# Performance work log

Hardware: AMD Instinct MI355X
Metric: run time of the kernel (lower is better)

The kernel has to match this reference:

```python
import jax, jax.numpy as jnp
import numpy as np

N, D = 4096, 512
TAU, ALPHA, EPS = 0.2, 0.5, 1e-15
L2_EPS = 1e-12  # F.normalize eps


def setup_inputs() -> dict:
    key = jax.random.key(0)
    ks = jax.random.split(key, 12)
    # xavier_normal_ with gain=1.414 for [D, D] linears
    std = 1.414 * (2.0 / (D + D)) ** 0.5
    xn = lambda k: jax.random.normal(k, (D, D), jnp.float32) * std
    return {
        "z1": jax.random.normal(ks[0], (N, D), jnp.float32),
        "z2": jax.random.normal(ks[1], (N, D), jnp.float32),
        # local projector: Linear -> PReLU -> Linear
        "lw1": xn(ks[2]), "lb1": jnp.zeros((D,), jnp.float32),
        "la": jnp.full((1,), 0.25, jnp.float32),  # PReLU weight (torch default 0.25)
        "lw2": xn(ks[3]), "lb2": jnp.zeros((D,), jnp.float32),
        # global projector
        "gw1": xn(ks[4]), "gb1": jnp.zeros((D,), jnp.float32),
        "ga": jnp.full((1,), 0.25, jnp.float32),
        "gw2": xn(ks[5]), "gb2": jnp.zeros((D,), jnp.float32),
        # discriminator bilinear weight
        "W": xn(ks[6]),
        # binary positive-pair mask [N, N]
        "mask": jax.random.randint(ks[7], (N, N), 0, 2, jnp.int32),
    }


def _prelu(x, a):
    return jnp.where(x >= 0, x, a * x)


def _proj(z, w1, b1, a, w2, b2):
    # nn.Sequential(Linear, PReLU, Linear); torch Linear: z @ W.T + b
    return _prelu(z @ w1.T + b1, a[0]) @ w2.T + b2


def _l2norm(z):
    n = jnp.linalg.norm(z, axis=-1, keepdims=True)
    return z / jnp.maximum(n, L2_EPS)


def _infonce(h1, h2, m, tau):
    a = _l2norm(h1)
    b = _l2norm(h2)
    sim_intra = jnp.exp(a @ a.T / tau)  # [N, N]
    sim_inter = jnp.exp(a @ b.T / tau)  # [N, N]
    num = (sim_inter * m).sum(1)
    den = sim_intra.sum(1) + sim_inter.sum(1) - (sim_intra * m).sum(1)
    return (-jnp.log(num / den)).mean()


def reference(z1, z2, lw1, lb1, la, lw2, lb2, gw1, gb1, ga, gw2, gb2, W, mask):
    m = mask.astype(jnp.float32)
    # local (node-level) InfoNCE through the local projector
    h1 = _proj(z1, lw1, lb1, la, lw2, lb2)
    h2 = _proj(z2, lw1, lb1, la, lw2, lb2)
    local = 0.5 * (_infonce(h1, h2, m, TAU) + _infonce(h2, h1, m.T, TAU))

    # global (DGI-style) loss
    def gloss(pos_z, neg_z):
        s = pos_z.mean(0)                               # readout [D]
        h = _proj(s, gw1, gb1, ga, gw2, gb2)            # global projector [D]
        summ = W @ h                                    # [D]
        d_pos = jax.nn.sigmoid(pos_z @ summ)            # [N]
        d_neg = jax.nn.sigmoid(neg_z @ summ)            # [N]
        pos_loss = -jnp.log(d_pos + EPS).mean()
        neg_loss = -jnp.log(1.0 - d_neg + EPS).mean()
        return 0.5 * (pos_loss + neg_loss)

    glob = 0.5 * (gloss(z1, z2) + gloss(z2, z1))
    return ALPHA * local + (1.0 - ALPHA) * glob
```

## Files before the change

### kernel.cpp

```cpp
#include <hip/hip_runtime.h>
#include <math.h>

#define NN 4096
#define DD 512
#define INV_TAU 5.0f
#define EPSV 1e-15f

typedef unsigned short u16;
typedef __attribute__((ext_vector_type(8))) short short8;
typedef __attribute__((ext_vector_type(4))) float f32x4;

__device__ __forceinline__ void gld16(const void* g, void* l) {
  __builtin_amdgcn_global_load_lds(
      (const __attribute__((address_space(1))) unsigned int*)g,
      (__attribute__((address_space(3))) unsigned int*)l, 16, 0, 0);
}

__device__ __forceinline__ float bf2f(u16 u) {
  return __uint_as_float(((unsigned)u) << 16);
}
__device__ __forceinline__ u16 f2bf(float x) {
  unsigned u = __float_as_uint(x);
  u += 0x7fff + ((u >> 16) & 1);
  return (u16)(u >> 16);
}

__device__ __forceinline__ float wave_sum(float v) {
#pragma unroll
  for (int o = 32; o > 0; o >>= 1) v += __shfl_down(v, o, 64);
  return v;
}

__global__ __launch_bounds__(256) void tobf16_2(const float* __restrict__ a,
                                                const float* __restrict__ b,
                                                u16* __restrict__ d,
                                                int n4each) {
  const int i = blockIdx.x * 256 + threadIdx.x;
  const float* s =
      (i < n4each) ? a + (size_t)i * 4 : b + (size_t)(i - n4each) * 4;
  float4 v = *(const float4*)s;
  unsigned long long pk = (unsigned long long)f2bf(v.x) |
                          ((unsigned long long)f2bf(v.y) << 16) |
                          ((unsigned long long)f2bf(v.z) << 32) |
                          ((unsigned long long)f2bf(v.w) << 48);
  *(unsigned long long*)&d[(size_t)i * 4] = pk;
}

template <int ACT>
__global__ __launch_bounds__(256) void gemm_mfma(
    const u16* __restrict__ A, const u16* __restrict__ Bw,
    const float* __restrict__ bias, const float* __restrict__ alpha_p,
    u16* __restrict__ out) {
  __shared__ __align__(16) u16 sA[2][128 * 32], sB[2][128 * 32];
  const int tid = threadIdx.x, w = tid >> 6, lane = tid & 63;
  const int rq = lane >> 2, cq = (lane & 3) * 8;
  const int quad = lane >> 4, m16 = lane & 15;
  const int wi = w >> 1, wj = w & 1;
  const int i0 = blockIdx.y * 128, j0 = blockIdx.x * 128;
  const u16* Ab = A + (size_t)blockIdx.z * ((size_t)NN * DD);
  u16* ob = out + (size_t)blockIdx.z * ((size_t)NN * DD);
  const int p = w >> 1, rh = (w & 1) * 64;
  const u16* gs = p ? Bw : Ab;
  const int grow0 = (p ? j0 : i0) + rh + rq;
  u16* lb0 = p ? &sB[0][rh * 32] : &sA[0][rh * 32];
  u16* lb1 = p ? &sB[1][rh * 32] : &sA[1][rh * 32];
#pragma unroll
  for (int rr = 0; rr < 64; rr += 16)
    gld16(&gs[(size_t)(grow0 + rr) * DD + cq], lb0 + rr * 32);
  f32x4 acc[4][4] = {};
  for (int kc = 0; kc < 16; ++kc) {
    __syncthreads();
    if (kc < 15) {
      const int kn = (kc + 1) * 32;
      u16* d = (kc & 1) ? lb0 : lb1;
#pragma unroll
      for (int rr = 0; rr < 64; rr += 16)
        gld16(&gs[(size_t)(grow0 + rr) * DD + kn + cq], d + rr * 32);
    }
    const u16* As = sA[kc & 1];
    const u16* Bs = sB[kc & 1];
    short8 ar[4], br[4];
#pragma unroll
    for (int s = 0; s < 4; ++s) {
      ar[s] = *(const short8*)&As[(wi * 64 + s * 16 + m16) * 32 + quad * 8];
      br[s] = *(const short8*)&Bs[(wj * 64 + s * 16 + m16) * 32 + quad * 8];
    }
#pragma unroll
    for (int si = 0; si < 4; ++si)
#pragma unroll
      for (int sj = 0; sj < 4; ++sj)
        acc[si][sj] = __builtin_amdgcn_mfma_f32_16x16x32_bf16(
            ar[si], br[sj], acc[si][sj], 0, 0, 0);
  }
  const float al = ACT ? alpha_p[0] : 0.f;
#pragma unroll
  for (int si = 0; si < 4; ++si)
#pragma unroll
    for (int sj = 0; sj < 4; ++sj) {
      const int col = j0 + wj * 64 + sj * 16 + m16;
      const float bv = bias[col];
#pragma unroll
      for (int r = 0; r < 4; ++r) {
        const int row = i0 + wi * 64 + si * 16 + quad * 4 + r;
        float x = acc[si][sj][r] + bv;
        if (ACT) x = (x >= 0.f) ? x : al * x;
        ob[(size_t)row * DD + col] = f2bf(x);
      }
    }
}

__global__ __launch_bounds__(256) void rownorm_bf16(const u16* __restrict__ h,
                                                    u16* __restrict__ o) {
  const int row = blockIdx.x;
  const int t = threadIdx.x;
  const size_t base = (size_t)row * DD;
  float v0 = bf2f(h[base + t]);
  float v1 = bf2f(h[base + 256 + t]);
  float s = v0 * v0 + v1 * v1;
  s = wave_sum(s);
  __shared__ float wsum[4];
  const int lane = t & 63, wid = t >> 6;
  if (lane == 0) wsum[wid] = s;
  __syncthreads();
  if (t == 0) {
    float tot = wsum[0] + wsum[1] + wsum[2] + wsum[3];
    wsum[0] = 1.f / fmaxf(sqrtf(tot), 1e-12f);
  }
  __syncthreads();
  const float inv = wsum[0];
  o[base + t] = f2bf(v0 * inv);
  o[base + 256 + t] = f2bf(v1 * inv);
}

__global__ __launch_bounds__(512) void sim_mfma(
    const u16* __restrict__ na, const u16* __restrict__ nb,
    const int* __restrict__ mask, float* __restrict__ zb) {
  __shared__ __align__(16) u16 sP[2][4][128 * 32];
  const int tid = threadIdx.x;
  const int w = tid >> 6, lane = tid & 63;
  const int rq = lane >> 2, cq = (lane & 3) * 8;
  const int quad = lane >> 4, m16 = lane & 15;
  const int ig = w & 3, jh = w >> 2;
  const int i0 = blockIdx.y * 128, j0 = blockIdx.x * 128;
  const int p = w >> 1, rh = (w & 1) * 64;
  const u16* gs = (p & 1) ? nb : na;
  const int grow0 = ((p < 2) ? i0 : j0) + rh + rq;
  u16* lb0 = &sP[0][p][rh * 32];
  u16* lb1 = &sP[1][p][rh * 32];
#pragma unroll
  for (int rr = 0; rr < 64; rr += 16)
    gld16(&gs[(size_t)(grow0 + rr) * DD + cq], lb0 + rr * 32);
  f32x4 a11[2][4] = {}, a12[2][4] = {}, a22[2][4] = {};
  for (int kc = 0; kc < 16; ++kc) {
    __syncthreads();
    if (kc < 15) {
      const int kn = (kc + 1) * 32;
      u16* d = (kc & 1) ? lb0 : lb1;
#pragma unroll
      for (int rr = 0; rr < 64; rr += 16)
        gld16(&gs[(size_t)(grow0 + rr) * DD + kn + cq], d + rr * 32);
    }
    const u16* Ai = sP[kc & 1][0];
    const u16* Bi = sP[kc & 1][1];
    const u16* Aj = sP[kc & 1][2];
    const u16* Bj = sP[kc & 1][3];
    short8 ai0 = *(const short8*)&Ai[(ig * 32 + m16) * 32 + quad * 8];
    short8 ai1 = *(const short8*)&Ai[(ig * 32 + 16 + m16) * 32 + quad * 8];
    short8 bi0 = *(const short8*)&Bi[(ig * 32 + m16) * 32 + quad * 8];
    short8 bi1 = *(const short8*)&Bi[(ig * 32 + 16 + m16) * 32 + quad * 8];
#pragma unroll
    for (int c = 0; c < 4; ++c) {
      short8 aj = *(const short8*)&Aj[(jh * 64 + c * 16 + m16) * 32 + quad * 8];
      short8 bj = *(const short8*)&Bj[(jh * 64 + c * 16 + m16) * 32 + quad * 8];
      a11[0][c] = __builtin_amdgcn_mfma_f32_16x16x32_bf16(ai0, aj, a11[0][c], 0, 0, 0);
      a11[1][c] = __builtin_amdgcn_mfma_f32_16x16x32_bf16(ai1, aj, a11[1][c], 0, 0, 0);
      a12[0][c] = __builtin_amdgcn_mfma_f32_16x16x32_bf16(ai0, bj, a12[0][c], 0, 0, 0);
      a12[1][c] = __builtin_amdgcn_mfma_f32_16x16x32_bf16(ai1, bj, a12[1][c], 0, 0, 0);
      a22[0][c] = __builtin_amdgcn_mfma_f32_16x16x32_bf16(bi0, bj, a22[0][c], 0, 0, 0);
      a22[1][c] = __builtin_amdgcn_mfma_f32_16x16x32_bf16(bi1, bj, a22[1][c], 0, 0, 0);
    }
  }
  float* rred = (float*)&sP[0][0][0];
  float* cred = rred + 512;
  rred[tid] = 0.f;
  rred[tid + 512] = 0.f;
  __syncthreads();
  float rs11[2][4] = {}, rm11[2][4] = {}, rs12[2][4] = {}, rm12[2][4] = {};
  float cs12[4] = {}, cm12[4] = {}, cs22[4] = {}, cm22[4] = {};
#pragma unroll
  for (int t = 0; t < 2; ++t)
#pragma unroll
    for (int c = 0; c < 4; ++c) {
      const int gj = j0 + jh * 64 + c * 16 + m16;
#pragma unroll
      for (int r = 0; r < 4; ++r) {
        const int gi = i0 + ig * 32 + t * 16 + quad * 4 + r;
        const float mv = (float)mask[(size_t)gi * NN + gj];
        const float e11 = __expf(a11[t][c][r] * INV_TAU);
        const float e12 = __expf(a12[t][c][r] * INV_TAU);
        const float e22 = __expf(a22[t][c][r] * INV_TAU);
        rs11[t][r] += e11;
        rm11[t][r] += e11 * mv;
        rs12[t][r] += e12;
        rm12[t][r] += e12 * mv;
        cs12[c] += e12;
        cm12[c] += e12 * mv;
        cs22[c] += e22;
        cm22[c] += e22 * mv;
      }
    }
#pragma unroll
  for (int t = 0; t < 2; ++t)
#pragma unroll
    for (int r = 0; r < 4; ++r) {
      float v0 = rs11[t][r], v1 = rm11[t][r], v2 = rs12[t][r], v3 = rm12[t][r];
#pragma unroll
      for (int o = 1; o < 16; o <<= 1) {
        v0 += __shfl_xor(v0, o, 64);
        v1 += __shfl_xor(v1, o, 64);
        v2 += __shfl_xor(v2, o, 64);
        v3 += __shfl_xor(v3, o, 64);
      }
      if (m16 == 0) {
        const int il = ig * 32 + t * 16 + quad * 4 + r;
        atomicAdd(&rred[0 * 128 + il], v0);
        atomicAdd(&rred[1 * 128 + il], v1);
        atomicAdd(&rred[2 * 128 + il], v2);
        atomicAdd(&rred[3 * 128 + il], v3);
      }
    }
#pragma unroll
  for (int c = 0; c < 4; ++c) {
    float v0 = cs12[c], v1 = cm12[c], v2 = cs22[c], v3 = cm22[c];
    v0 += __shfl_xor(v0, 16, 64); v0 += __shfl_xor(v0, 32, 64);
    v1 += __shfl_xor(v1, 16, 64); v1 += __shfl_xor(v1, 32, 64);
    v2 += __shfl_xor(v2, 16, 64); v2 += __shfl_xor(v2, 32, 64);
    v3 += __shfl_xor(v3, 16, 64); v3 += __shfl_xor(v3, 32, 64);
    if (lane < 16) {
      const int jl = jh * 64 + c * 16 + lane;
      atomicAdd(&cred[0 * 128 + jl], v0);
      atomicAdd(&cred[1 * 128 + jl], v1);
      atomicAdd(&cred[2 * 128 + jl], v2);
      atomicAdd(&cred[3 * 128 + jl], v3);
    }
  }
  __syncthreads();
  if (tid < 128) {
#pragma unroll
    for (int q = 0; q < 4; ++q)
      atomicAdd(&zb[q * NN + i0 + tid], rred[q * 128 + tid]);
  } else if (tid < 256) {
    const int jl = tid - 128;
#pragma unroll
    for (int q = 0; q < 4; ++q)
      atomicAdd(&zb[(4 + q) * NN + j0 + jl], cred[q * 128 + jl]);
  }
}

__global__ __launch_bounds__(256) void local_fin(const float* __restrict__ zb,
                                                 float* __restrict__ scal) {
  const int i = blockIdx.x * 256 + threadIdx.x;
  const float r11 = zb[i], r11m = zb[NN + i];
  const float r12 = zb[2 * NN + i], r12m = zb[3 * NN + i];
  const float c12 = zb[4 * NN + i], c12m = zb[5 * NN + i];
  const float c22 = zb[6 * NN + i], c22m = zb[7 * NN + i];
  float l1 = -logf(r12m / (r11 + r12 - r11m));
  float l2 = -logf(c12m / (c22 + c12 - c22m));
  l1 = wave_sum(l1);
  l2 = wave_sum(l2);
  __shared__ float b1[4], b2[4];
  const int lane = threadIdx.x & 63, wid = threadIdx.x >> 6;
  if (lane == 0) { b1[wid] = l1; b2[wid] = l2; }
  __syncthreads();
  if (threadIdx.x == 0) {
    atomicAdd(&scal[0], b1[0] + b1[1] + b1[2] + b1[3]);
    atomicAdd(&scal[1], b2[0] + b2[1] + b2[2] + b2[3]);
  }
}

__global__ __launch_bounds__(256) void colmean(const float* __restrict__ z1,
                                               const float* __restrict__ z2,
                                               float* __restrict__ s1,
                                               float* __restrict__ s2) {
  const int c = blockIdx.x * 256 + threadIdx.x;
  const int r0 = blockIdx.y * 64;
  float a = 0.f, b = 0.f;
  for (int r = r0; r < r0 + 64; ++r) {
    a += z1[(size_t)r * DD + c];
    b += z2[(size_t)r * DD + c];
  }
  atomicAdd(&s1[c], a * (1.f / NN));
  atomicAdd(&s2[c], b * (1.f / NN));
}

__global__ __launch_bounds__(256) void matvec2(
    const float* __restrict__ M, const float* __restrict__ x1,
    const float* __restrict__ x2, const float* __restrict__ bias,
    const float* __restrict__ alpha_p, int act, float* __restrict__ y1,
    float* __restrict__ y2) {
  const float* x = blockIdx.y ? x2 : x1;
  float* y = blockIdx.y ? y2 : y1;
  const int row = (blockIdx.x * 256 + threadIdx.x) >> 6;
  const int lane = threadIdx.x & 63;
  float acc = 0.f;
#pragma unroll
  for (int t = 0; t < 8; ++t)
    acc = fmaf(M[(size_t)row * DD + lane + 64 * t], x[lane + 64 * t], acc);
  acc = wave_sum(acc);
  if (lane == 0) {
    if (bias) acc += bias[row];
    if (act) { const float al = alpha_p[0]; acc = (acc >= 0.f) ? acc : al * acc; }
    y[row] = acc;
  }
}

__global__ __launch_bounds__(256) void logsig2(
    const float* __restrict__ z1, const float* __restrict__ z2,
    const float* __restrict__ sm1, const float* __restrict__ sm2,
    float* __restrict__ scal) {
  const int ch = blockIdx.y;
  const float* z = ch ? z2 : z1;
  const float* sp = ch ? sm2 : sm1;
  const float* sn = ch ? sm1 : sm2;
  float* accP = ch ? &scal[4] : &scal[2];
  float* accN = ch ? &scal[3] : &scal[5];
  const int lane = threadIdx.x & 63;
  const int wid = threadIdx.x >> 6;
  const int row = blockIdx.x * 4 + wid;
  float dp = 0.f, dn = 0.f;
#pragma unroll
  for (int t = 0; t < 8; ++t) {
    const float zv = z[(size_t)row * DD + lane + 64 * t];
    dp = fmaf(zv, sp[lane + 64 * t], dp);
    dn = fmaf(zv, sn[lane + 64 * t], dn);
  }
  dp = wave_sum(dp);
  dn = wave_sum(dn);
  __shared__ float bp[4], bn[4];
  if (lane == 0) {
    const float sg = 1.f / (1.f + __expf(-dp));
    bp[wid] = -logf(sg + EPSV);
    const float sg2 = 1.f / (1.f + __expf(-dn));
    bn[wid] = -logf(1.f - sg2 + EPSV);
  }
  __syncthreads();
  if (threadIdx.x == 0) {
    atomicAdd(accP, bp[0] + bp[1] + bp[2] + bp[3]);
    atomicAdd(accN, bn[0] + bn[1] + bn[2] + bn[3]);
  }
}

__global__ void combine(const float* __restrict__ scal, float* __restrict__ out) {
  const float local = 0.5f * (scal[0] + scal[1]) * (1.f / NN);
  const float glob = 0.25f * (scal[2] + scal[3] + scal[4] + scal[5]) * (1.f / NN);
  out[0] = 0.5f * local + 0.5f * glob;
}

extern "C" void kernel_launch(void* const* d_in, const int* in_sizes, int n_in,
                              void* d_out, int out_size, void* d_ws,
                              size_t ws_size, hipStream_t stream) {
  const float* z1 = (const float*)d_in[0];
  const float* z2 = (const float*)d_in[1];
  const float* lw1 = (const float*)d_in[2];
  const float* lb1 = (const float*)d_in[3];
  const float* la = (const float*)d_in[4];
  const float* lw2 = (const float*)d_in[5];
  const float* lb2 = (const float*)d_in[6];
  const float* gw1 = (const float*)d_in[7];
  const float* gb1 = (const float*)d_in[8];
  const float* ga = (const float*)d_in[9];
  const float* gw2 = (const float*)d_in[10];
  const float* gb2 = (const float*)d_in[11];
  const float* W = (const float*)d_in[12];
  const int* mask = (const int*)d_in[13];
  float* out = (float*)d_out;

  const size_t ND = (size_t)NN * DD;
  u16* W1b = (u16*)d_ws;
  u16* W2b = W1b + 512 * 512;
  u16* Ab = W1b + 2 * 512 * 512;
  u16* Bb = Ab + 2 * ND;
  float* zbf = (float*)(Bb + 2 * ND);
  float* s1 = zbf + 8 * NN;
  float* s2 = s1 + DD;
  float* scal = s2 + DD;
  float* t1 = scal + 16;
  float* hg1 = t1 + DD;
  float* summ1 = hg1 + DD;
  float* t2 = summ1 + DD;
  float* hg2 = t2 + DD;
  float* summ2 = hg2 + DD;

  hipMemsetAsync(zbf, 0, (8 * NN + 2 * DD + 16) * sizeof(float), stream);

  dim3 blk(256);
  tobf16_2<<<512, blk, 0, stream>>>(lw1, lw2, W1b, 512 * 512 / 4);
  tobf16_2<<<4096, blk, 0, stream>>>(z1, z2, Ab, (int)(ND / 4));

  dim3 gg(4, 32, 2);
  gemm_mfma<1><<<gg, blk, 0, stream>>>(Ab, W1b, lb1, la, Bb);
  gemm_mfma<0><<<gg, blk, 0, stream>>>(Bb, W2b, lb2, la, Ab);
  rownorm_bf16<<<2 * NN, blk, 0, stream>>>(Ab, Bb);

  sim_mfma<<<dim3(NN / 128, NN / 128), dim3(512), 0, stream>>>(Bb, Bb + ND,
                                                               mask, zbf);
  local_fin<<<NN / 256, blk, 0, stream>>>(zbf, scal);

  colmean<<<dim3(DD / 256, 64), blk, 0, stream>>>(z1, z2, s1, s2);
  matvec2<<<dim3(DD / 4, 2), blk, 0, stream>>>(gw1, s1, s2, gb1, ga, 1, t1, t2);
  matvec2<<<dim3(DD / 4, 2), blk, 0, stream>>>(gw2, t1, t2, gb2, nullptr, 0, hg1, hg2);
  matvec2<<<dim3(DD / 4, 2), blk, 0, stream>>>(W, hg1, hg2, nullptr, nullptr, 0, summ1, summ2);
  logsig2<<<dim3(NN / 4, 2), blk, 0, stream>>>(z1, z2, summ1, summ2, scal);

  combine<<<1, 1, 0, stream>>>(scal, out);
}
```

Before: 309.5 us.

## Triple-buffer LDS staging with swizzled layout and priority hints in MFMA GEMMs

Both the projector GEMM and the similarity kernel move from double to triple buffering. Tiles are prefetched two k-steps ahead, and the __syncthreads is replaced by a partial vmcnt wait plus barrier, so global-to-LDS loads overlap more compute. The LDS layout is XOR-swizzled on both the store and read side to reduce bank conflicts, and s_setprio raises wave priority around the MFMA blocks. The sim kernel now uses 96KB of dynamic LDS, which may lower occupancy.

```diff
diff --git a/kernel.cpp b/kernel.cpp
--- a/kernel.cpp
+++ b/kernel.cpp
@@ -14,6 +14,13 @@
   __builtin_amdgcn_global_load_lds(
       (const __attribute__((address_space(1))) unsigned int*)g,
       (__attribute__((address_space(3))) unsigned int*)l, 16, 0, 0);
+}
+
+__device__ __forceinline__ void bar_vm4() {
+  asm volatile("s_waitcnt vmcnt(4) lgkmcnt(0)\n\ts_barrier" ::: "memory");
+}
+__device__ __forceinline__ void bar_vm0() {
+  asm volatile("s_waitcnt vmcnt(0) lgkmcnt(0)\n\ts_barrier" ::: "memory");
 }
 
 __device__ __forceinline__ float bf2f(u16 u) {
@@ -51,46 +58,59 @@
     const u16* __restrict__ A, const u16* __restrict__ Bw,
     const float* __restrict__ bias, const float* __restrict__ alpha_p,
     u16* __restrict__ out) {
-  __shared__ __align__(16) u16 sA[2][128 * 32], sB[2][128 * 32];
+  __shared__ __align__(16) u16 sh[3 * 2 * 128 * 32];
   const int tid = threadIdx.x, w = tid >> 6, lane = tid & 63;
-  const int rq = lane >> 2, cq = (lane & 3) * 8;
   const int quad = lane >> 4, m16 = lane & 15;
   const int wi = w >> 1, wj = w & 1;
   const int i0 = blockIdx.y * 128, j0 = blockIdx.x * 128;
   const u16* Ab = A + (size_t)blockIdx.z * ((size_t)NN * DD);
   u16* ob = out + (size_t)blockIdx.z * ((size_t)NN * DD);
+  const int roff =
+      (m16 >> 1) * 64 + (((((m16 & 1) << 2) | quad) ^ (m16 >> 1)) * 8);
+  const int st = (lane & 7) ^ (lane >> 3);
+  const int srow = 2 * (lane >> 3) + (st >> 2);
+  const int scol = (st & 3) * 8;
   const int p = w >> 1, rh = (w & 1) * 64;
   const u16* gs = p ? Bw : Ab;
-  const int grow0 = (p ? j0 : i0) + rh + rq;
-  u16* lb0 = p ? &sB[0][rh * 32] : &sA[0][rh * 32];
-  u16* lb1 = p ? &sB[1][rh * 32] : &sA[1][rh * 32];
-#pragma unroll
-  for (int rr = 0; rr < 64; rr += 16)
-    gld16(&gs[(size_t)(grow0 + rr) * DD + cq], lb0 + rr * 32);
+  const int gr = (p ? j0 : i0) + rh + srow;
+  u16* dst0 = sh + p * 4096 + rh * 32;
+  auto stage = [&](int bo, int k) {
+    const int kn = k * 32;
+#pragma unroll
+    for (int rr = 0; rr < 64; rr += 16)
+      gld16(&gs[(size_t)(gr + rr) * DD + kn + scol], dst0 + bo + rr * 32);
+  };
+  stage(0, 0);
+  stage(8192, 1);
+  bar_vm4();
   f32x4 acc[4][4] = {};
+  int ro = 0;
   for (int kc = 0; kc < 16; ++kc) {
-    __syncthreads();
-    if (kc < 15) {
-      const int kn = (kc + 1) * 32;
-      u16* d = (kc & 1) ? lb0 : lb1;
-#pragma unroll
-      for (int rr = 0; rr < 64; rr += 16)
-        gld16(&gs[(size_t)(grow0 + rr) * DD + kn + cq], d + rr * 32);
-    }
-    const u16* As = sA[kc & 1];
-    const u16* Bs = sB[kc & 1];
+    if (kc <= 13) {
+      int so = ro + 16384;
+      if (so >= 24576) so -= 24576;
+      stage(so, kc + 2);
+    }
+    const u16* As = sh + ro;
+    const u16* Bs = sh + ro + 4096;
     short8 ar[4], br[4];
 #pragma unroll
     for (int s = 0; s < 4; ++s) {
-      ar[s] = *(const short8*)&As[(wi * 64 + s * 16 + m16) * 32 + quad * 8];
-      br[s] = *(const short8*)&Bs[(wj * 64 + s * 16 + m16) * 32 + quad * 8];
-    }
+      ar[s] = *(const short8*)&As[(wi * 64 + s * 16) * 32 + roff];
+      br[s] = *(const short8*)&Bs[(wj * 64 + s * 16) * 32 + roff];
+    }
+    __builtin_amdgcn_s_setprio(1);
 #pragma unroll
     for (int si = 0; si < 4; ++si)
 #pragma unroll
       for (int sj = 0; sj < 4; ++sj)
         acc[si][sj] = __builtin_amdgcn_mfma_f32_16x16x32_bf16(
             ar[si], br[sj], acc[si][sj], 0, 0, 0);
+    __builtin_amdgcn_s_setprio(0);
+    if (kc <= 13) bar_vm4();
+    else if (kc == 14) bar_vm0();
+    ro += 8192;
+    if (ro == 24576) ro = 0;
   }
   const float al = ACT ? alpha_p[0] : 0.f;
 #pragma unroll
@@ -135,52 +155,65 @@
 __global__ __launch_bounds__(512) void sim_mfma(
     const u16* __restrict__ na, const u16* __restrict__ nb,
     const int* __restrict__ mask, float* __restrict__ zb) {
-  __shared__ __align__(16) u16 sP[2][4][128 * 32];
+  extern __shared__ __align__(16) u16 shm[];
   const int tid = threadIdx.x;
   const int w = tid >> 6, lane = tid & 63;
-  const int rq = lane >> 2, cq = (lane & 3) * 8;
   const int quad = lane >> 4, m16 = lane & 15;
   const int ig = w & 3, jh = w >> 2;
   const int i0 = blockIdx.y * 128, j0 = blockIdx.x * 128;
+  const int roff =
+      (m16 >> 1) * 64 + (((((m16 & 1) << 2) | quad) ^ (m16 >> 1)) * 8);
+  const int st = (lane & 7) ^ (lane >> 3);
+  const int srow = 2 * (lane >> 3) + (st >> 2);
+  const int scol = (st & 3) * 8;
   const int p = w >> 1, rh = (w & 1) * 64;
   const u16* gs = (p & 1) ? nb : na;
-  const int grow0 = ((p < 2) ? i0 : j0) + rh + rq;
-  u16* lb0 = &sP[0][p][rh * 32];
-  u16* lb1 = &sP[1][p][rh * 32];
-#pragma unroll
-  for (int rr = 0; rr < 64; rr += 16)
-    gld16(&gs[(size_t)(grow0 + rr) * DD + cq], lb0 + rr * 32);
+  const int gr = ((p < 2) ? i0 : j0) + rh + srow;
+  u16* dst0 = shm + p * 4096 + rh * 32;
+  auto stage = [&](int bo, int k) {
+    const int kn = k * 32;
+#pragma unroll
+    for (int rr = 0; rr < 64; rr += 16)
+      gld16(&gs[(size_t)(gr + rr) * DD + kn + scol], dst0 + bo + rr * 32);
+  };
+  stage(0, 0);
+  stage(16384, 1);
+  bar_vm4();
   f32x4 a11[2][4] = {}, a12[2][4] = {}, a22[2][4] = {};
+  int ro = 0;
   for (int kc = 0; kc < 16; ++kc) {
-    __syncthreads();
-    if (kc < 15) {
-      const int kn = (kc + 1) * 32;
-      u16* d = (kc & 1) ? lb0 : lb1;
-#pragma unroll
-      for (int rr = 0; rr < 64; rr += 16)
-        gld16(&gs[(size_t)(grow0 + rr) * DD + kn + cq], d + rr * 32);
-    }
-    const u16* Ai = sP[kc & 1][0];
-    const u16* Bi = sP[kc & 1][1];
-    const u16* Aj = sP[kc & 1][2];
-    const u16* Bj = sP[kc & 1][3];
-    short8 ai0 = *(const short8*)&Ai[(ig * 32 + m16) * 32 + quad * 8];
-    short8 ai1 = *(const short8*)&Ai[(ig * 32 + 16 + m16) * 32 + quad * 8];
-    short8 bi0 = *(const short8*)&Bi[(ig * 32 + m16) * 32 + quad * 8];
-    short8 bi1 = *(const short8*)&Bi[(ig * 32 + 16 + m16) * 32 + quad * 8];
+    if (kc <= 13) {
+      int so = ro + 32768;
+      if (so >= 49152) so -= 49152;
+      stage(so, kc + 2);
+    }
+    const u16* Ai = shm + ro;
+    const u16* Bi = shm + ro + 4096;
+    const u16* Aj = shm + ro + 8192;
+    const u16* Bj = shm + ro + 12288;
+    short8 ai0 = *(const short8*)&Ai[(ig * 32) * 32 + roff];
+    short8 ai1 = *(const short8*)&Ai[(ig * 32 + 16) * 32 + roff];
+    short8 bi0 = *(const short8*)&Bi[(ig * 32) * 32 + roff];
+    short8 bi1 = *(const short8*)&Bi[(ig * 32 + 16) * 32 + roff];
 #pragma unroll
     for (int c = 0; c < 4; ++c) {
-      short8 aj = *(const short8*)&Aj[(jh * 64 + c * 16 + m16) * 32 + quad * 8];
-      short8 bj = *(const short8*)&Bj[(jh * 64 + c * 16 + m16) * 32 + quad * 8];
+      short8 aj = *(const short8*)&Aj[(jh * 64 + c * 16) * 32 + roff];
+      short8 bj = *(const short8*)&Bj[(jh * 64 + c * 16) * 32 + roff];
+      __builtin_amdgcn_s_setprio(1);
       a11[0][c] = __builtin_amdgcn_mfma_f32_16x16x32_bf16(ai0, aj, a11[0][c], 0, 0, 0);
       a11[1][c] = __builtin_amdgcn_mfma_f32_16x16x32_bf16(ai1, aj, a11[1][c], 0, 0, 0);
       a12[0][c] = __builtin_amdgcn_mfma_f32_16x16x32_bf16(ai0, bj, a12[0][c], 0, 0, 0);
       a12[1][c] = __builtin_amdgcn_mfma_f32_16x16x32_bf16(ai1, bj, a12[1][c], 0, 0, 0);
       a22[0][c] = __builtin_amdgcn_mfma_f32_16x16x32_bf16(bi0, bj, a22[0][c], 0, 0, 0);
       a22[1][c] = __builtin_amdgcn_mfma_f32_16x16x32_bf16(bi1, bj, a22[1][c], 0, 0, 0);
-    }
-  }
-  float* rred = (float*)&sP[0][0][0];
+      __builtin_amdgcn_s_setprio(0);
+    }
+    if (kc <= 13) bar_vm4();
+    else if (kc == 14) bar_vm0();
+    ro += 16384;
+    if (ro == 49152) ro = 0;
+  }
+  float* rred = (float*)(shm + 16384);
   float* cred = rred + 512;
   rred[tid] = 0.f;
   rred[tid + 512] = 0.f;
@@ -375,6 +408,14 @@
   const int* mask = (const int*)d_in[13];
   float* out = (float*)d_out;
 
+  static bool attr_set = false;
+  if (!attr_set) {
+    (void)hipFuncSetAttribute(reinterpret_cast<const void*>(sim_mfma),
+                              hipFuncAttributeMaxDynamicSharedMemorySize,
+                              98304);
+    attr_set = true;
+  }
+
   const size_t ND = (size_t)NN * DD;
   u16* W1b = (u16*)d_ws;
   u16* W2b = W1b + 512 * 512;
@@ -402,8 +443,8 @@
   gemm_mfma<0><<<gg, blk, 0, stream>>>(Bb, W2b, lb2, la, Ab);
   rownorm_bf16<<<2 * NN, blk, 0, stream>>>(Ab, Bb);
 
-  sim_mfma<<<dim3(NN / 128, NN / 128), dim3(512), 0, stream>>>(Bb, Bb + ND,
-                                                               mask, zbf);
+  sim_mfma<<<dim3(NN / 128, NN / 128), dim3(512), 98304, stream>>>(
+      Bb, Bb + ND, mask, zbf);
   local_fin<<<NN / 256, blk, 0, stream>>>(zbf, scal);
 
   colmean<<<dim3(DD / 256, 64), blk, 0, stream>>>(z1, z2, s1, s2);
```

Result: no change. 310.2 us (+0.2%).
